# Kernel tuning notes

Hardware: AMD Instinct MI355X
Metric: run time of the kernel (lower is better)

The kernel has to match this reference:

```python
import jax, jax.numpy as jnp
import numpy as np

D_MODEL = 1024
N_HEADS = 16
HEAD_DIM = 64
D_FF = 4096


def rmsnorm(x, w):
    eps = jnp.finfo(x.dtype).eps
    var = jnp.mean(jnp.square(x), axis=-1, keepdims=True)
    return x * jax.lax.rsqrt(var + eps) * w


def setup_inputs() -> dict:
    key = jax.random.key(0)
    ks = jax.random.split(key, 8)
    d, h, hd, dff = D_MODEL, N_HEADS, HEAD_DIM, D_FF
    s = 0.02
    return {
        "x": jax.random.normal(ks[0], (2, 2048, d), dtype=jnp.float32),
        "norm_w": jnp.ones((d,), dtype=jnp.float32),
        "Wq": jax.random.normal(ks[1], (d, h * hd), dtype=jnp.float32) * s,
        "Wk": jax.random.normal(ks[2], (d, h * hd), dtype=jnp.float32) * s,
        "Wv": jax.random.normal(ks[3], (d, h * hd), dtype=jnp.float32) * s,
        "Wo": jax.random.normal(ks[4], (h * hd, d), dtype=jnp.float32) * s,
        "W1": jax.random.normal(ks[5], (d, dff), dtype=jnp.float32) * s,
        "W2": jax.random.normal(ks[6], (dff, d), dtype=jnp.float32) * s,
    }


def reference(x, norm_w, Wq, Wk, Wv, Wo, W1, W2):
    B, T, d = x.shape
    h, hd = N_HEADS, HEAD_DIM
    scale = 1.0 / np.sqrt(hd)

    xn = rmsnorm(x, norm_w)

    # attention branch
    q = (xn @ Wq).reshape(B, T, h, hd).transpose(0, 2, 1, 3)  # [B,h,T,hd]
    k = (xn @ Wk).reshape(B, T, h, hd).transpose(0, 2, 1, 3)
    v = (xn @ Wv).reshape(B, T, h, hd).transpose(0, 2, 1, 3)
    attn = jnp.einsum("bhqd,bhkd->bhqk", q, k) * scale
    causal = jnp.tril(jnp.ones((T, T), dtype=bool))
    attn = jnp.where(causal, attn, -jnp.inf)
    attn = jax.nn.softmax(attn, axis=-1)
    out = jnp.einsum("bhqk,bhkd->bhqd", attn, v)
    out = out.transpose(0, 2, 1, 3).reshape(B, T, h * hd)
    attn_out = out @ Wo

    # FFN branch
    ffn_out = jax.nn.silu(xn @ W1) @ W2

    return x + attn_out + ffn_out
```

## Files before the change

### kernel.cpp

```cpp
#include <hip/hip_runtime.h>

#define DM   1024
#define DFF  4096
#define NH   16
#define HD   64
#define TT   2048
#define BT   4096
#define KC   5120

typedef unsigned short u16;
typedef unsigned int   u32;
typedef __attribute__((ext_vector_type(8))) short s16x8;
typedef __attribute__((ext_vector_type(4))) float f32x4;

__device__ __forceinline__ u16 f2bf(float f) {
  u32 u = __builtin_bit_cast(u32, f);
  u += 0x7fffu + ((u >> 16) & 1u);
  return (u16)(u >> 16);
}

__device__ __forceinline__ void gl2lds16(const void* g, void* l) {
  __builtin_amdgcn_global_load_lds((__attribute__((address_space(1))) void*)(g),
                                   (__attribute__((address_space(3))) void*)(l),
                                   16, 0, 0);
}

#define S_BARRIER() do { __builtin_amdgcn_s_barrier(); __builtin_amdgcn_sched_barrier(0); } while (0)
#define VMWAIT(n)   asm volatile("s_waitcnt vmcnt(" #n ")" ::: "memory")

__global__ __launch_bounds__(256) void rmsnorm_k(const float* __restrict__ x,
                                                 const float* __restrict__ w,
                                                 u16* __restrict__ xn) {
  const int row = blockIdx.x;
  const int t = threadIdx.x;
  const float4 v = ((const float4*)(x + (size_t)row * DM))[t];
  float ss = v.x*v.x + v.y*v.y + v.z*v.z + v.w*v.w;
  #pragma unroll
  for (int off = 32; off; off >>= 1) ss += __shfl_xor(ss, off, 64);
  __shared__ float red[4];
  if ((t & 63) == 0) red[t >> 6] = ss;
  __syncthreads();
  const float tot = red[0] + red[1] + red[2] + red[3];
  const float r = __builtin_amdgcn_rsqf(tot * (1.0f / DM) + 1.1920929e-7f);
  const float4 wv = ((const float4*)w)[t];
  u16* o = xn + (size_t)row * DM + t * 4;
  o[0] = f2bf(v.x * r * wv.x);
  o[1] = f2bf(v.y * r * wv.y);
  o[2] = f2bf(v.z * r * wv.z);
  o[3] = f2bf(v.w * r * wv.w);
}

__global__ __launch_bounds__(256) void wtrans_k(const float* __restrict__ W,
                                                u16* __restrict__ Wt,
                                                int K, int N, int pitch, int koff) {
  __shared__ float tile[32][33];
  const int n0 = blockIdx.x * 32, k0 = blockIdx.y * 32;
  const int tx = threadIdx.x, ty = threadIdx.y;
  #pragma unroll
  for (int i = 0; i < 4; ++i)
    tile[ty + i*8][tx] = W[(size_t)(k0 + ty + i*8) * N + n0 + tx];
  __syncthreads();
  #pragma unroll
  for (int i = 0; i < 4; ++i)
    Wt[(size_t)(n0 + ty + i*8) * pitch + koff + k0 + tx] = f2bf(tile[tx][ty + i*8]);
}

__global__ __launch_bounds__(512, 2) void gemm_fused(const u16* __restrict__ A,
                                                     const u16* __restrict__ Bt,
                                                     u16* __restrict__ qkb,
                                                     u16* __restrict__ vtg,
                                                     u16* __restrict__ acat) {
  const int K = 1024;
  __shared__ u16 sA[2 * 16384];
  __shared__ u16 sB[2 * 16384];
  const int t = threadIdx.x;
  const int lane = t & 63, wave = t >> 6;
  const int quad = lane >> 4, l4 = lane & 15;
  const int wy = wave >> 2, wx = wave & 3;
  const size_t mBase = (size_t)blockIdx.y * 256;
  const size_t nBase = (size_t)blockIdx.x * 256;

  const int grow = t >> 3;
  const int gchk = ((t & 7) ^ (grow & 7)) * 8;
  const u16* AgR = A  + (mBase + grow) * K + gchk;
  const u16* BgR = Bt + (nBase + grow) * K + gchk;
  char* dA = (char*)sA;
  char* dB = (char*)sB;
  const int woff = wave * 1024;

  const int cs0 = ((quad)     ^ (l4 & 7)) * 8;
  const int cs1 = ((4 + quad) ^ (l4 & 7)) * 8;

  f32x4 acc[8][4];
  #pragma unroll
  for (int i = 0; i < 8; ++i)
    #pragma unroll
    for (int j = 0; j < 4; ++j)
      acc[i][j] = (f32x4)0.0f;

  s16x8 a[4][2], b[4][2];

  #define STG(p, slot, kt) do {                                                  \
    const int k0_ = (kt) * 64;                                                   \
    if ((p) == 0) {                                                              \
      gl2lds16(BgR + (size_t)0*64*K + k0_, dB + (slot)*32768 +     0 + woff);    \
      gl2lds16(BgR + (size_t)1*64*K + k0_, dB + (slot)*32768 +  8192 + woff);    \
    } else if ((p) == 1) {                                                       \
      gl2lds16(BgR + (size_t)2*64*K + k0_, dB + (slot)*32768 + 16384 + woff);    \
      gl2lds16(BgR + (size_t)3*64*K + k0_, dB + (slot)*32768 + 24576 + woff);    \
    } else if ((p) == 2) {                                                       \
      gl2lds16(AgR + (size_t)0*64*K + k0_, dA + (slot)*32768 +     0 + woff);    \
      gl2lds16(AgR + (size_t)2*64*K + k0_, dA + (slot)*32768 + 16384 + woff);    \
    } else {                                                                     \
      gl2lds16(AgR + (size_t)1*64*K + k0_, dA + (slot)*32768 +  8192 + woff);    \
      gl2lds16(AgR + (size_t)3*64*K + k0_, dA + (slot)*32768 + 24576 + woff);    \
    }                                                                            \
  } while (0)

  #define RDA(slot, qm) do {                                                     \
    const u16* p_ = sA + (slot)*16384 + wy*8192;                                 \
    _Pragma("unroll")                                                            \
    for (int m_ = 0; m_ < 4; ++m_) {                                             \
      const int ro_ = (((qm)*4 + m_)*16 + l4) * 64;                              \
      a[m_][0] = *(const s16x8*)&p_[ro_ + cs0];                                  \
      a[m_][1] = *(const s16x8*)&p_[ro_ + cs1];                                  \
    }                                                                            \
  } while (0)

  #define RDB(slot, qn) do {                                                     \
    const u16* p_ = sB + (slot)*16384 + (wx>>1)*8192 + (wx&1)*4096;              \
    _Pragma("unroll")                                                            \
    for (int n_ = 0; n_ < 2; ++n_) {                                             \
      const int ro_ = (((qn)*2 + n_)*16 + l4) * 64;                              \
      b[(qn)*2 + n_][0] = *(const s16x8*)&p_[ro_ + cs0];                         \
      b[(qn)*2 + n_][1] = *(const s16x8*)&p_[ro_ + cs1];                         \
    }                                                                            \
  } while (0)

  #define MM(qm, qn) do {                                                        \
    __builtin_amdgcn_s_setprio(1);                                               \
    _Pragma("unroll")                                                            \
    for (int m_ = 0; m_ < 4; ++m_)                                               \
      _Pragma("unroll")                                                          \
      for (int n_ = 0; n_ < 2; ++n_) {                                           \
        acc[(qm)*4+m_][(qn)*2+n_] = __builtin_amdgcn_mfma_f32_16x16x32_bf16(     \
            a[m_][0], b[(qn)*2+n_][0], acc[(qm)*4+m_][(qn)*2+n_], 0, 0, 0);      \
        acc[(qm)*4+m_][(qn)*2+n_] = __builtin_amdgcn_mfma_f32_16x16x32_bf16(     \
            a[m_][1], b[(qn)*2+n_][1], acc[(qm)*4+m_][(qn)*2+n_], 0, 0, 0);      \
      }                                                                          \
    __builtin_amdgcn_s_setprio(0);                                               \
  } while (0)

  STG(0, 0, 0); STG(1, 0, 0); STG(2, 0, 0); STG(3, 0, 0);
  VMWAIT(2);
  S_BARRIER();

  for (int i = 0; i < 7; ++i) {
    const int kt1 = 2*i + 1, kt2 = 2*i + 2;
    RDA(0,0); RDB(0,0); STG(0,1,kt1); S_BARRIER(); MM(0,0);            S_BARRIER();
    RDB(0,1);           STG(1,1,kt1); S_BARRIER(); MM(0,1); VMWAIT(4); S_BARRIER();
    RDA(0,1);           STG(2,1,kt1); S_BARRIER(); MM(1,0);            S_BARRIER();
                        STG(3,1,kt1); S_BARRIER(); MM(1,1); VMWAIT(2); S_BARRIER();
    RDA(1,0); RDB(1,0); STG(0,0,kt2); S_BARRIER(); MM(0,0);            S_BARRIER();
    RDB(1,1);           STG(1,0,kt2); S_BARRIER(); MM(0,1); VMWAIT(4); S_BARRIER();
    RDA(1,1);           STG(2,0,kt2); S_BARRIER(); MM(1,0);            S_BARRIER();
                        STG(3,0,kt2); S_BARRIER(); MM(1,1); VMWAIT(2); S_BARRIER();
  }
  RDA(0,0); RDB(0,0); STG(0,1,15); S_BARRIER(); MM(0,0);            S_BARRIER();
  RDB(0,1);           STG(1,1,15); S_BARRIER(); MM(0,1); VMWAIT(4); S_BARRIER();
  RDA(0,1);           STG(2,1,15); S_BARRIER(); MM(1,0);            S_BARRIER();
                      STG(3,1,15); S_BARRIER(); MM(1,1); VMWAIT(2); S_BARRIER();
  RDA(1,0); RDB(1,0);              S_BARRIER(); MM(0,0);            S_BARRIER();
  RDB(1,1);                        S_BARRIER(); MM(0,1); VMWAIT(0); S_BARRIER();
  RDA(1,1);                        S_BARRIER(); MM(1,0);            S_BARRIER();
                                   S_BARRIER(); MM(1,1);            S_BARRIER();

  #undef STG
  #undef RDA
  #undef RDB
  #undef MM

  #pragma unroll
  for (int i = 0; i < 8; ++i) {
    const size_t row0 = mBase + wy*128 + i*16 + quad*4;
    #pragma unroll
    for (int j = 0; j < 4; ++j) {
      const int col = (int)nBase + wx*64 + j*16 + l4;
      if (nBase < 1024) {
        #pragma unroll
        for (int rg = 0; rg < 4; ++rg)
          qkb[(row0 + rg) * 2048 + col] = f2bf(acc[i][j][rg] * 0.18033688011f);
      } else if (nBase < 2048) {
        #pragma unroll
        for (int rg = 0; rg < 4; ++rg)
          qkb[(row0 + rg) * 2048 + col] = f2bf(acc[i][j][rg]);
      } else if (nBase < 3072) {
        const int cv = col - 2048, hh = cv >> 6, dd = cv & 63;
        const int bb = (int)(row0 >> 11), t0 = (int)(row0 & 2047);
        ushort4 pk;
        pk.x = f2bf(acc[i][j][0]); pk.y = f2bf(acc[i][j][1]);
        pk.z = f2bf(acc[i][j][2]); pk.w = f2bf(acc[i][j][3]);
        *(ushort4*)(vtg + ((size_t)((bb*16 + hh)*64 + dd)) * 2048 + t0) = pk;
      } else {
        #pragma unroll
        for (int rg = 0; rg < 4; ++rg) {
          float v = acc[i][j][rg];
          v = v / (1.0f + __expf(-v));
          acat[(row0 + rg) * (size_t)KC + 1024 + (col - 3072)] = f2bf(v);
        }
      }
    }
  }
}

__global__ __launch_bounds__(256, 2) void gemm_final(const u16* __restrict__ A,
                                                     const u16* __restrict__ Bt,
                                                     const float* __restrict__ x,
                                                     float* __restrict__ out) {
  __shared__ u16 sA[6 * 64 * 32];
  __shared__ u16 sB[6 * 128 * 32];
  const int t = threadIdx.x;
  const int lane = t & 63, wave = t >> 6;
  const int quad = lane >> 4, l4 = lane & 15;
  const int wy = wave >> 1, wx = wave & 1;
  const int d  = blockIdx.x + (blockIdx.y << 3);
  const int vb = ((d & 7) << 6) | (d >> 3);
  const int bx = vb & 7, by = vb >> 3;
  const size_t mBase = (size_t)by * 64;
  const size_t nBase = (size_t)bx * 128;
  const int r  = t >> 2;
  const int c8 = ((t & 3) ^ ((t >> 3) & 3)) * 8;
  const int qsw = (quad ^ ((l4 >> 1) & 3)) * 8;
  const u16* Ag  = A  + (mBase + r) * KC + c8;
  const u16* Bg0 = Bt + (nBase + r) * KC + c8;
  const u16* Bg1 = Bg0 + (size_t)64 * KC;
  char* sAb = (char*)sA + (wave << 10);
  char* sBb = (char*)sB + (wave << 10);

  f32x4 acc[2][4];
  #pragma unroll
  for (int i = 0; i < 2; ++i)
    #pragma unroll
    for (int j = 0; j < 4; ++j)
      acc[i][j] = (f32x4)0.0f;

  auto issue = [&](int sl, int k0) {
    gl2lds16(Ag  + k0, sAb + sl*4096);
    gl2lds16(Bg0 + k0, sBb + sl*8192);
    gl2lds16(Bg1 + k0, sBb + sl*8192 + 4096);
  };

  auto compute = [&](int sl) {
    const u16* pA = sA + sl * 2048;
    const u16* pB = sB + sl * 4096;
    s16x8 af[2], bfr[4];
    #pragma unroll
    for (int i = 0; i < 2; ++i)
      af[i] = *(const s16x8*)&pA[(wy*32 + i*16 + l4) * 32 + qsw];
    #pragma unroll
    for (int j = 0; j < 4; ++j)
      bfr[j] = *(const s16x8*)&pB[(wx*64 + j*16 + l4) * 32 + qsw];
    #pragma unroll
    for (int i = 0; i < 2; ++i)
      #pragma unroll
      for (int j = 0; j < 4; ++j)
        acc[i][j] = __builtin_amdgcn_mfma_f32_16x16x32_bf16(af[i], bfr[j], acc[i][j], 0, 0, 0);
  };

  const int NIT = KC / 32;
  issue(0, 0); issue(1, 32); issue(2, 64); issue(3, 96); issue(4, 128);
  int sl = 0;
  for (int kt = 0; kt < NIT - 5; ++kt) {
    VMWAIT(12);
    S_BARRIER();
    issue(sl == 0 ? 5 : sl - 1, (kt + 5) * 32);
    compute(sl);
    sl = (sl == 5) ? 0 : sl + 1;
  }
  VMWAIT(12); S_BARRIER(); compute(sl); sl = (sl == 5) ? 0 : sl + 1;
  VMWAIT(9);  S_BARRIER(); compute(sl); sl = (sl == 5) ? 0 : sl + 1;
  VMWAIT(6);  S_BARRIER(); compute(sl); sl = (sl == 5) ? 0 : sl + 1;
  VMWAIT(3);  S_BARRIER(); compute(sl); sl = (sl == 5) ? 0 : sl + 1;
  VMWAIT(0);  S_BARRIER(); compute(sl);

  #pragma unroll
  for (int i = 0; i < 2; ++i) {
    const size_t row0 = mBase + wy*32 + i*16 + quad*4;
    #pragma unroll
    for (int j = 0; j < 4; ++j) {
      const int col = (int)nBase + wx*64 + j*16 + l4;
      #pragma unroll
      for (int rg = 0; rg < 4; ++rg) {
        const size_t idx = (row0 + rg) * (size_t)DM + col;
        out[idx] = x[idx] + acc[i][j][rg];
      }
    }
  }
}

__global__ __launch_bounds__(128) void attn_k(const u16* __restrict__ qk,
                                              const u16* __restrict__ vtg,
                                              u16* __restrict__ acat) {
  const int bh = blockIdx.x, b = bh >> 4, h = bh & 15;
  const int qt = 63 - blockIdx.y;
  const int qw = qt * 32;
  const int wave = threadIdx.x >> 6, lane = threadIdx.x & 63;
  const int quad = lane >> 4, l4 = lane & 15;
  const u16* Qp = qk + (size_t)b * TT * 2048 + h * HD;
  const u16* Kp = Qp + 1024;
  const u16* Vp = vtg + (size_t)bh * 64 * 2048;

  __shared__ u16 Pb[2][32][72];
  __shared__ float Ob[32][68];
  __shared__ float Lb[32];

  s16x8 qf[2][2];
  #pragma unroll
  for (int mi = 0; mi < 2; ++mi)
    #pragma unroll
    for (int kf = 0; kf < 2; ++kf)
      qf[mi][kf] = *(const s16x8*)(Qp + (size_t)(qw + mi*16 + l4) * 2048 + kf*32 + quad*8);

  const s16x8 ones = {0x3F80,0x3F80,0x3F80,0x3F80,0x3F80,0x3F80,0x3F80,0x3F80};

  f32x4 o[2][4];
  f32x4 lacc[2];
  #pragma unroll
  for (int mi = 0; mi < 2; ++mi) {
    lacc[mi] = (f32x4)0.0f;
    #pragma unroll
    for (int ni = 0; ni < 4; ++ni) o[mi][ni] = (f32x4)0.0f;
  }

  const int n   = (qt + 2) >> 1;
  const int n0  = (n + 1) >> 1;
  const int kt0 = wave ? n0 : 0;
  const int kt1 = wave ? n : n0;

  for (int kt = kt0; kt < kt1; ++kt) {
    const int k0 = kt * 64;

    f32x4 st[4][2];
    #pragma unroll
    for (int nj = 0; nj < 4; ++nj) {
      const u16* kr = Kp + (size_t)(k0 + nj*16 + l4) * 2048 + quad*8;
      const s16x8 kf0 = *(const s16x8*)kr;
      const s16x8 kf1 = *(const s16x8*)(kr + 32);
      #pragma unroll
      for (int mi = 0; mi < 2; ++mi) {
        f32x4 a = (f32x4)0.0f;
        a = __builtin_amdgcn_mfma_f32_16x16x32_bf16(kf0, qf[mi][0], a, 0, 0, 0);
        a = __builtin_amdgcn_mfma_f32_16x16x32_bf16(kf1, qf[mi][1], a, 0, 0, 0);
        st[nj][mi] = a;
      }
    }

    s16x8 vb[2][4];
    #pragma unroll
    for (int kf2 = 0; kf2 < 2; ++kf2)
      #pragma unroll
      for (int ni = 0; ni < 4; ++ni)
        vb[kf2][ni] = *(const s16x8*)(Vp + (size_t)(ni*16 + l4) * 2048 + k0 + kf2*32 + quad*8);

    if (k0 + 63 > qw) {
      #pragma unroll
      for (int nj = 0; nj < 4; ++nj)
        #pragma unroll
        for (int mi = 0; mi < 2; ++mi)
          #pragma unroll
          for (int rg = 0; rg < 4; ++rg) {
            const int key = k0 + nj*16 + quad*4 + rg;
            const int q   = qw + mi*16 + l4;
            if (key > q) st[nj][mi][rg] = -1e30f;
          }
    }

    #pragma unroll
    for (int nj = 0; nj < 4; ++nj)
      #pragma unroll
      for (int mi = 0; mi < 2; ++mi) {
        float p0 = __builtin_amdgcn_exp2f(st[nj][mi][0]);
        float p1 = __builtin_amdgcn_exp2f(st[nj][mi][1]);
        float p2 = __builtin_amdgcn_exp2f(st[nj][mi][2]);
        float p3 = __builtin_amdgcn_exp2f(st[nj][mi][3]);
        uint2 w;
        w.x = __builtin_amdgcn_perm(__builtin_bit_cast(u32, p1),
                                    __builtin_bit_cast(u32, p0), 0x07060302u);
        w.y = __builtin_amdgcn_perm(__builtin_bit_cast(u32, p3),
                                    __builtin_bit_cast(u32, p2), 0x07060302u);
        *(uint2*)&Pb[wave][mi*16 + l4][nj*16 + quad*4] = w;
      }

    #pragma unroll
    for (int kf2 = 0; kf2 < 2; ++kf2) {
      s16x8 pa[2];
      #pragma unroll
      for (int mi = 0; mi < 2; ++mi)
        pa[mi] = *(const s16x8*)&Pb[wave][mi*16 + l4][kf2*32 + quad*8];
      #pragma unroll
      for (int mi = 0; mi < 2; ++mi) {
        lacc[mi] = __builtin_amdgcn_mfma_f32_16x16x32_bf16(pa[mi], ones, lacc[mi], 0, 0, 0);
        #pragma unroll
        for (int ni = 0; ni < 4; ++ni)
          o[mi][ni] = __builtin_amdgcn_mfma_f32_16x16x32_bf16(pa[mi], vb[kf2][ni], o[mi][ni], 0, 0, 0);
      }
    }
  }

  if (wave == 1) {
    #pragma unroll
    for (int mi = 0; mi < 2; ++mi)
      #pragma unroll
      for (int rg = 0; rg < 4; ++rg) {
        const int row = mi*16 + quad*4 + rg;
        #pragma unroll
        for (int ni = 0; ni < 4; ++ni) Ob[row][ni*16 + l4] = o[mi][ni][rg];
        if (l4 == 0) Lb[row] = lacc[mi][rg];
      }
  }
  __syncthreads();
  if (wave == 0) {
    #pragma unroll
    for (int mi = 0; mi < 2; ++mi)
      #pragma unroll
      for (int rg = 0; rg < 4; ++rg) {
        const int row = mi*16 + quad*4 + rg;
        const float inv = 1.0f / (lacc[mi][rg] + Lb[row]);
        #pragma unroll
        for (int ni = 0; ni < 4; ++ni)
          Pb[0][row][ni*16 + l4] = f2bf((o[mi][ni][rg] + Ob[row][ni*16 + l4]) * inv);
      }
    #pragma unroll
    for (int it = 0; it < 4; ++it) {
      const int row = it*8 + (lane >> 3);
      const int c0  = (lane & 7) * 8;
      const s16x8 pk = *(const s16x8*)&Pb[0][row][c0];
      *(s16x8*)(acat + ((size_t)b * TT + qw + row) * KC + h*HD + c0) = pk;
    }
  }
}

extern "C" void kernel_launch(void* const* d_in, const int* in_sizes, int n_in,
                              void* d_out, int out_size, void* d_ws, size_t ws_size,
                              hipStream_t stream) {
  (void)in_sizes; (void)n_in; (void)out_size; (void)ws_size;
  const float* x  = (const float*)d_in[0];
  const float* nw = (const float*)d_in[1];
  const float* Wq = (const float*)d_in[2];
  const float* Wk = (const float*)d_in[3];
  const float* Wv = (const float*)d_in[4];
  const float* Wo = (const float*)d_in[5];
  const float* W1 = (const float*)d_in[6];
  const float* W2 = (const float*)d_in[7];

  char* ws = (char*)d_ws;
  u16*   xn      = (u16*)(ws);
  u16*   wqkv1_t = (u16*)(ws + ((size_t)8  << 20));
  u16*   bcat    = (u16*)(ws + ((size_t)22 << 20));
  u16*   qkb     = (u16*)(ws + ((size_t)32 << 20));
  u16*   vtg     = (u16*)(ws + ((size_t)48 << 20));
  u16*   acat    = (u16*)(ws + ((size_t)56 << 20));
  float* dout    = (float*)d_out;

  rmsnorm_k<<<BT, 256, 0, stream>>>(x, nw, xn);
  const dim3 tb(32, 8);
  wtrans_k<<<dim3(32, 32),  tb, 0, stream>>>(Wq, wqkv1_t,                      1024, 1024, 1024, 0);
  wtrans_k<<<dim3(32, 32),  tb, 0, stream>>>(Wk, wqkv1_t + (size_t)1024*1024,  1024, 1024, 1024, 0);
  wtrans_k<<<dim3(32, 32),  tb, 0, stream>>>(Wv, wqkv1_t + (size_t)2048*1024,  1024, 1024, 1024, 0);
  wtrans_k<<<dim3(128, 32), tb, 0, stream>>>(W1, wqkv1_t + (size_t)3072*1024,  1024, 4096, 1024, 0);
  wtrans_k<<<dim3(32, 32),  tb, 0, stream>>>(Wo, bcat,                         1024, 1024, 5120, 0);
  wtrans_k<<<dim3(32, 128), tb, 0, stream>>>(W2, bcat,                         4096, 1024, 5120, 1024);

  gemm_fused<<<dim3(28, 16), 512, 0, stream>>>(xn, wqkv1_t, qkb, vtg, acat);
  attn_k<<<dim3(32, 64), 128, 0, stream>>>(qkb, vtg, acat);
  gemm_final<<<dim3(8, 64), 256, 0, stream>>>(acat, bcat, x, dout);
}
```

Baseline: 365.8 us.

## Split-K the final GEMM with atomic accumulation into a pre-seeded residual output

```diff
diff --git a/kernel.cpp b/kernel.cpp
--- a/kernel.cpp
+++ b/kernel.cpp
@@ -30,10 +30,12 @@
 
 __global__ __launch_bounds__(256) void rmsnorm_k(const float* __restrict__ x,
                                                  const float* __restrict__ w,
-                                                 u16* __restrict__ xn) {
+                                                 u16* __restrict__ xn,
+                                                 float* __restrict__ outx) {
   const int row = blockIdx.x;
   const int t = threadIdx.x;
   const float4 v = ((const float4*)(x + (size_t)row * DM))[t];
+  ((float4*)(outx + (size_t)row * DM))[t] = v;
   float ss = v.x*v.x + v.y*v.y + v.z*v.z + v.w*v.w;
   #pragma unroll
   for (int off = 32; off; off >>= 1) ss += __shfl_xor(ss, off, 64);
@@ -213,12 +215,11 @@
   }
 }
 
-__global__ __launch_bounds__(256, 2) void gemm_final(const u16* __restrict__ A,
+__global__ __launch_bounds__(256, 4) void gemm_final(const u16* __restrict__ A,
                                                      const u16* __restrict__ Bt,
-                                                     const float* __restrict__ x,
                                                      float* __restrict__ out) {
-  __shared__ u16 sA[6 * 64 * 32];
-  __shared__ u16 sB[6 * 128 * 32];
+  __shared__ u16 sA[3 * 64 * 32];
+  __shared__ u16 sB[3 * 128 * 32];
   const int t = threadIdx.x;
   const int lane = t & 63, wave = t >> 6;
   const int quad = lane >> 4, l4 = lane & 15;
@@ -228,11 +229,12 @@
   const int bx = vb & 7, by = vb >> 3;
   const size_t mBase = (size_t)by * 64;
   const size_t nBase = (size_t)bx * 128;
+  const int kBase = (int)blockIdx.z * 2560;
   const int r  = t >> 2;
   const int c8 = ((t & 3) ^ ((t >> 3) & 3)) * 8;
   const int qsw = (quad ^ ((l4 >> 1) & 3)) * 8;
-  const u16* Ag  = A  + (mBase + r) * KC + c8;
-  const u16* Bg0 = Bt + (nBase + r) * KC + c8;
+  const u16* Ag  = A  + (mBase + r) * KC + kBase + c8;
+  const u16* Bg0 = Bt + (nBase + r) * KC + kBase + c8;
   const u16* Bg1 = Bg0 + (size_t)64 * KC;
   char* sAb = (char*)sA + (wave << 10);
   char* sBb = (char*)sB + (wave << 10);
@@ -267,21 +269,16 @@
         acc[i][j] = __builtin_amdgcn_mfma_f32_16x16x32_bf16(af[i], bfr[j], acc[i][j], 0, 0, 0);
   };
 
-  const int NIT = KC / 32;
-  issue(0, 0); issue(1, 32); issue(2, 64); issue(3, 96); issue(4, 128);
-  int sl = 0;
-  for (int kt = 0; kt < NIT - 5; ++kt) {
-    VMWAIT(12);
+  const int NIT = 2560 / 32;
+  issue(0, 0); issue(1, 32);
+  for (int kt = 0; kt < NIT - 2; ++kt) {
+    VMWAIT(3);
     S_BARRIER();
-    issue(sl == 0 ? 5 : sl - 1, (kt + 5) * 32);
-    compute(sl);
-    sl = (sl == 5) ? 0 : sl + 1;
-  }
-  VMWAIT(12); S_BARRIER(); compute(sl); sl = (sl == 5) ? 0 : sl + 1;
-  VMWAIT(9);  S_BARRIER(); compute(sl); sl = (sl == 5) ? 0 : sl + 1;
-  VMWAIT(6);  S_BARRIER(); compute(sl); sl = (sl == 5) ? 0 : sl + 1;
-  VMWAIT(3);  S_BARRIER(); compute(sl); sl = (sl == 5) ? 0 : sl + 1;
-  VMWAIT(0);  S_BARRIER(); compute(sl);
+    issue((kt + 2) % 3, (kt + 2) * 32);
+    compute(kt % 3);
+  }
+  VMWAIT(3); S_BARRIER(); compute((NIT - 2) % 3);
+  VMWAIT(0); S_BARRIER(); compute((NIT - 1) % 3);
 
   #pragma unroll
   for (int i = 0; i < 2; ++i) {
@@ -290,10 +287,8 @@
     for (int j = 0; j < 4; ++j) {
       const int col = (int)nBase + wx*64 + j*16 + l4;
       #pragma unroll
-      for (int rg = 0; rg < 4; ++rg) {
-        const size_t idx = (row0 + rg) * (size_t)DM + col;
-        out[idx] = x[idx] + acc[i][j][rg];
-      }
+      for (int rg = 0; rg < 4; ++rg)
+        atomicAdd(out + (row0 + rg) * (size_t)DM + col, acc[i][j][rg]);
     }
   }
 }
@@ -462,7 +457,7 @@
   u16*   acat    = (u16*)(ws + ((size_t)56 << 20));
   float* dout    = (float*)d_out;
 
-  rmsnorm_k<<<BT, 256, 0, stream>>>(x, nw, xn);
+  rmsnorm_k<<<BT, 256, 0, stream>>>(x, nw, xn, dout);
   const dim3 tb(32, 8);
   wtrans_k<<<dim3(32, 32),  tb, 0, stream>>>(Wq, wqkv1_t,                      1024, 1024, 1024, 0);
   wtrans_k<<<dim3(32, 32),  tb, 0, stream>>>(Wk, wqkv1_t + (size_t)1024*1024,  1024, 1024, 1024, 0);
@@ -473,5 +468,5 @@
 
   gemm_fused<<<dim3(28, 16), 512, 0, stream>>>(xn, wqkv1_t, qkb, vtg, acat);
   attn_k<<<dim3(32, 64), 128, 0, stream>>>(qkb, vtg, acat);
-  gemm_final<<<dim3(8, 64), 256, 0, stream>>>(acat, bcat, x, dout);
-}
+  gemm_final<<<dim3(8, 64, 2), 256, 0, stream>>>(acat, bcat, dout);
+}
```

Result: faster. 355.8 us (-2.7%).
